# Kernel tuning notes

Measured on AMD Instinct MI355X. Metric: run time of the kernel, lower is better.

Reference implementation:

```python
import jax, jax.numpy as jnp
import numpy as np

SQRT2 = np.float32(np.sqrt(2.0))
D = 256


def setup_inputs() -> dict:
    key = jax.random.key(0)
    k1, = jax.random.split(key, 1)
    x = jax.random.normal(k1, (4, 1024, D), dtype=jnp.float32)
    weight = jnp.ones((D,), dtype=jnp.float32)
    bias = jnp.zeros((D,), dtype=jnp.float32)
    return {"x": x, "weight": weight, "bias": bias}


def reference(x, weight, bias):
    orig_shape = x.shape
    d = orig_shape[-1]
    flat = x.reshape(-1, d)  # [N, D]
    # Silverman 2d bandwidth: 0.9 * std(ddof=1, dim=-1) * D^(-1/5)
    bw = 0.9 * jnp.std(flat, axis=-1, ddof=1) * np.float32(d ** (-0.2))  # [N]
    # Pairwise Gaussian-kernel CDF, averaged over data points (dim 2).
    scaled = (flat[:, :, None] - flat[:, None, :]) / bw[:, None, None]  # [N, D, D]
    cdf = jnp.mean(0.5 * (1.0 + jax.lax.erf(scaled / SQRT2)), axis=2)  # [N, D]
    # Gaussian PPF (inverse CDF)
    normed = jax.lax.erf_inv(2.0 * cdf - 1.0) * SQRT2  # [N, D]
    out = normed.reshape(orig_shape) * weight + bias
    return out
```

## Files before the change

kernel.cpp:

```cpp
#include <hip/hip_runtime.h>
#include <math.h>

#define DD 256
#define NW 4
#define MFIX 24

typedef float v2f __attribute__((ext_vector_type(2)));
typedef float v4f __attribute__((ext_vector_type(4)));

template <int CTRL>
__device__ __forceinline__ float dpp_add(float x) {
    return x + __int_as_float(__builtin_amdgcn_update_dpp(
        0, __float_as_int(x), CTRL, 0xf, 0xf, false));
}
template <int CTRL>
__device__ __forceinline__ float dpp_mov_self(float x) {
    return __int_as_float(__builtin_amdgcn_update_dpp(
        __float_as_int(x), __float_as_int(x), CTRL, 0xf, 0xf, false));
}
__device__ __forceinline__ float wave_sum_chain(float x) {
    x = dpp_add<0x111>(x); x = dpp_add<0x112>(x);
    x = dpp_add<0x114>(x); x = dpp_add<0x118>(x);
    x = dpp_add<0x142>(x); x = dpp_add<0x143>(x);
    return x;
}
__device__ __forceinline__ float lane63(float x) {
    return __int_as_float(__builtin_amdgcn_readlane(__float_as_int(x), 63));
}
__device__ __forceinline__ float wave_max_chain(float x) {
    x = __builtin_fmaxf(x, dpp_mov_self<0x111>(x));
    x = __builtin_fmaxf(x, dpp_mov_self<0x112>(x));
    x = __builtin_fmaxf(x, dpp_mov_self<0x114>(x));
    x = __builtin_fmaxf(x, dpp_mov_self<0x118>(x));
    x = __builtin_fmaxf(x, dpp_mov_self<0x142>(x));
    x = __builtin_fmaxf(x, dpp_mov_self<0x143>(x));
    return x;
}
__device__ __forceinline__ float wave_min_chain(float x) {
    x = __builtin_fminf(x, dpp_mov_self<0x111>(x));
    x = __builtin_fminf(x, dpp_mov_self<0x112>(x));
    x = __builtin_fminf(x, dpp_mov_self<0x114>(x));
    x = __builtin_fminf(x, dpp_mov_self<0x118>(x));
    x = __builtin_fminf(x, dpp_mov_self<0x142>(x));
    x = __builtin_fminf(x, dpp_mov_self<0x143>(x));
    return x;
}

__device__ __forceinline__ float ppf_from_y(float y) {
    float omy2 = __builtin_fmaf(-y, y, 1.0f);
    float wg = __builtin_fmaf(-__builtin_amdgcn_logf(omy2), 0.69314718056f, -2.5f);
    float p = 2.81022636e-08f;
    p = __builtin_fmaf(p, wg, 3.43273939e-07f);
    p = __builtin_fmaf(p, wg, -3.5233877e-06f);
    p = __builtin_fmaf(p, wg, -4.39150654e-06f);
    p = __builtin_fmaf(p, wg, 0.00021858087f);
    p = __builtin_fmaf(p, wg, -0.00125372503f);
    p = __builtin_fmaf(p, wg, -0.00417768164f);
    p = __builtin_fmaf(p, wg, 0.246640727f);
    p = __builtin_fmaf(p, wg, 1.50140941f);
    return p * y * 1.41421356237309505f;
}

__global__ __launch_bounds__(64 * NW, 4) void kd_layernorm_kernel(
        const float* __restrict__ x,
        const float* __restrict__ wgt,
        const float* __restrict__ bia,
        float* __restrict__ out) {
    const int lane = threadIdx.x & 63;
    const int wid  = threadIdx.x >> 6;
    const int row  = blockIdx.x * NW + wid;

    const v4f u = ((const v4f*)(x + (size_t)row * DD))[lane];

    float ssum = lane63(wave_sum_chain((u.x + u.y) + (u.z + u.w)));
    float qsum = lane63(wave_sum_chain(__builtin_fmaf(u.x, u.x, u.y * u.y) +
                                       __builtin_fmaf(u.z, u.z, u.w * u.w)));
    float xmax = lane63(wave_max_chain(__builtin_fmaxf(__builtin_fmaxf(u.x, u.y),
                                                       __builtin_fmaxf(u.z, u.w))));
    float xmin = lane63(wave_min_chain(__builtin_fminf(__builtin_fminf(u.x, u.y),
                                                       __builtin_fminf(u.z, u.w))));

    float var = (qsum - ssum * ssum * (1.0f / DD)) * (1.0f / (DD - 1));
    float bw = 0.9f * __builtin_sqrtf(var) * 0.32987697769322355f;
    float invbw = __builtin_amdgcn_rcpf(bw);
    v4f v = u * invbw;
    float meanv = ssum * invbw * (1.0f / DD);

    float L = (xmax - xmin) * invbw + 10.0f;
    float invL = __builtin_amdgcn_rcpf(L);

    v4f ph = v * invL;
    v4f s1, c1;
    s1.x = __builtin_amdgcn_sinf(ph.x); s1.y = __builtin_amdgcn_sinf(ph.y);
    s1.z = __builtin_amdgcn_sinf(ph.z); s1.w = __builtin_amdgcn_sinf(ph.w);
    c1.x = __builtin_amdgcn_cosf(ph.x); c1.y = __builtin_amdgcn_cosf(ph.y);
    c1.z = __builtin_amdgcn_cosf(ph.z); c1.w = __builtin_amdgcn_cosf(ph.w);

    float PC[MFIX], PS[MFIX];
    {
        v4f sm = s1, cm = c1;
        #pragma unroll
        for (int m = 0; m < MFIX; ++m) {
            PS[m] = (sm.x + sm.y) + (sm.z + sm.w);
            PC[m] = (cm.x + cm.y) + (cm.z + cm.w);
            v4f ns = __builtin_elementwise_fma(sm, c1, cm * s1);
            v4f nc = __builtin_elementwise_fma(cm, c1, -(sm * s1));
            sm = ns; cm = nc;
        }
    }

    {
        float w1sq = 39.4784176044f * invL * invL;
        float g   = __builtin_amdgcn_exp2f(-0.72134752f * w1sq);
        float rr  = __builtin_amdgcn_exp2f(-2.16404256f * w1sq);
        const float rho = __builtin_amdgcn_exp2f(-1.44269504f * w1sq);
        #pragma unroll
        for (int m = 0; m < MFIX; ++m) {
            float Ct = lane63(wave_sum_chain(PC[m]));
            float St = lane63(wave_sum_chain(PS[m]));
            float sc = g * (0.31830988618f / (float)(m + 1));
            PC[m] = Ct * sc;
            PS[m] = St * sc;
            g *= rr; rr *= rho;
        }
    }

    v4f R = {0.f, 0.f, 0.f, 0.f};
    {
        v4f sm = s1, cm = c1;
        #pragma unroll
        for (int m = 0; m < MFIX; ++m) {
            v4f vgC = {PC[m], PC[m], PC[m], PC[m]};
            v4f vgS = {PS[m], PS[m], PS[m], PS[m]};
            R = __builtin_elementwise_fma(sm, vgC, R);
            R = __builtin_elementwise_fma(cm, -vgS, R);
            v4f ns = __builtin_elementwise_fma(sm, c1, cm * s1);
            v4f nc = __builtin_elementwise_fma(cm, c1, -(sm * s1));
            sm = ns; cm = nc;
        }
    }

    const v4f wv = ((const v4f*)wgt)[lane];
    const v4f bv = ((const v4f*)bia)[lane];
    v4f o;
    o.x = __builtin_fmaf(ppf_from_y(2.0f * __builtin_fmaf(v.x - meanv, invL, R.x * (1.0f / DD))), wv.x, bv.x);
    o.y = __builtin_fmaf(ppf_from_y(2.0f * __builtin_fmaf(v.y - meanv, invL, R.y * (1.0f / DD))), wv.y, bv.y);
    o.z = __builtin_fmaf(ppf_from_y(2.0f * __builtin_fmaf(v.z - meanv, invL, R.z * (1.0f / DD))), wv.z, bv.z);
    o.w = __builtin_fmaf(ppf_from_y(2.0f * __builtin_fmaf(v.w - meanv, invL, R.w * (1.0f / DD))), wv.w, bv.w);
    ((v4f*)(out + (size_t)row * DD))[lane] = o;
}

extern "C" void kernel_launch(void* const* d_in, const int* in_sizes, int n_in,
                              void* d_out, int out_size, void* d_ws, size_t ws_size,
                              hipStream_t stream) {
    const float* x = (const float*)d_in[0];
    const float* w = (const float*)d_in[1];
    const float* b = (const float*)d_in[2];
    float* out = (float*)d_out;
    const int nrows = in_sizes[0] / DD;
    kd_layernorm_kernel<<<nrows / NW, 64 * NW, 0, stream>>>(x, w, b, out);
}
```

Measured before the change: 66.70 us.

## Use Chebyshev recurrence for harmonics and fuse reductions in groups for occupancy

Switches the angle-addition rotation for sin/cos harmonics to a Chebyshev three-term recurrence (one FMA per component, using 2cos). The per-harmonic scaling is folded into the first pass and the wave reductions run in groups of 8, so the separate scaling loop disappears and fewer values stay live. The constant factors (2/DD, sign) are also folded into the coefficients, and the launch bound is raised to 6 waves per SIMD to get more occupancy. The recurrence may build up more rounding error over 24 harmonics, and the tighter register budget could cause spills.

```diff
diff --git a/kernel.cpp b/kernel.cpp
--- a/kernel.cpp
+++ b/kernel.cpp
@@ -4,6 +4,7 @@
 #define DD 256
 #define NW 4
 #define MFIX 24
+#define MG 8
 
 typedef float v2f __attribute__((ext_vector_type(2)));
 typedef float v4f __attribute__((ext_vector_type(4)));
@@ -61,7 +62,7 @@
     return p * y * 1.41421356237309505f;
 }
 
-__global__ __launch_bounds__(64 * NW, 4) void kd_layernorm_kernel(
+__global__ __launch_bounds__(64 * NW, 6) void kd_layernorm_kernel(
         const float* __restrict__ x,
         const float* __restrict__ wgt,
         const float* __restrict__ bia,
@@ -95,58 +96,73 @@
     s1.z = __builtin_amdgcn_sinf(ph.z); s1.w = __builtin_amdgcn_sinf(ph.w);
     c1.x = __builtin_amdgcn_cosf(ph.x); c1.y = __builtin_amdgcn_cosf(ph.y);
     c1.z = __builtin_amdgcn_cosf(ph.z); c1.w = __builtin_amdgcn_cosf(ph.w);
+    v4f twoC = c1 + c1;
 
-    float PC[MFIX], PS[MFIX];
+    float w1sq = 39.4784176044f * invL * invL;
+    float g    = __builtin_amdgcn_exp2f(-0.72134752f * w1sq);
+    float rr   = __builtin_amdgcn_exp2f(-2.16404256f * w1sq);
+    const float rho = __builtin_amdgcn_exp2f(-1.44269504f * w1sq);
+
+    float gC[MFIX], gS[MFIX];
     {
         v4f sm = s1, cm = c1;
+        v4f sm1 = {0.f, 0.f, 0.f, 0.f};
+        v4f cm1 = {1.f, 1.f, 1.f, 1.f};
         #pragma unroll
-        for (int m = 0; m < MFIX; ++m) {
-            PS[m] = (sm.x + sm.y) + (sm.z + sm.w);
-            PC[m] = (cm.x + cm.y) + (cm.z + cm.w);
-            v4f ns = __builtin_elementwise_fma(sm, c1, cm * s1);
-            v4f nc = __builtin_elementwise_fma(cm, c1, -(sm * s1));
-            sm = ns; cm = nc;
-        }
-    }
-
-    {
-        float w1sq = 39.4784176044f * invL * invL;
-        float g   = __builtin_amdgcn_exp2f(-0.72134752f * w1sq);
-        float rr  = __builtin_amdgcn_exp2f(-2.16404256f * w1sq);
-        const float rho = __builtin_amdgcn_exp2f(-1.44269504f * w1sq);
-        #pragma unroll
-        for (int m = 0; m < MFIX; ++m) {
-            float Ct = lane63(wave_sum_chain(PC[m]));
-            float St = lane63(wave_sum_chain(PS[m]));
-            float sc = g * (0.31830988618f / (float)(m + 1));
-            PC[m] = Ct * sc;
-            PS[m] = St * sc;
-            g *= rr; rr *= rho;
-        }
-    }
-
-    v4f R = {0.f, 0.f, 0.f, 0.f};
-    {
-        v4f sm = s1, cm = c1;
-        #pragma unroll
-        for (int m = 0; m < MFIX; ++m) {
-            v4f vgC = {PC[m], PC[m], PC[m], PC[m]};
-            v4f vgS = {PS[m], PS[m], PS[m], PS[m]};
-            R = __builtin_elementwise_fma(sm, vgC, R);
-            R = __builtin_elementwise_fma(cm, -vgS, R);
-            v4f ns = __builtin_elementwise_fma(sm, c1, cm * s1);
-            v4f nc = __builtin_elementwise_fma(cm, c1, -(sm * s1));
-            sm = ns; cm = nc;
+        for (int grp = 0; grp < MFIX / MG; ++grp) {
+            float pc[MG], ps[MG];
+            #pragma unroll
+            for (int k = 0; k < MG; ++k) {
+                const int m = grp * MG + k;
+                float sc = g * (0.0024867959f / (float)(m + 1));
+                pc[k] = ((cm.x + cm.y) + (cm.z + cm.w)) * sc;
+                ps[k] = ((sm.x + sm.y) + (sm.z + sm.w)) * (-sc);
+                g *= rr; rr *= rho;
+                v4f sn = __builtin_elementwise_fma(twoC, sm, -sm1);
+                v4f cn = __builtin_elementwise_fma(twoC, cm, -cm1);
+                sm1 = sm; sm = sn;
+                cm1 = cm; cm = cn;
+            }
+            #pragma unroll
+            for (int k = 0; k < MG; ++k) {
+                const int m = grp * MG + k;
+                gC[m] = lane63(wave_sum_chain(pc[k]));
+                gS[m] = lane63(wave_sum_chain(ps[k]));
+            }
         }
     }
 
     const v4f wv = ((const v4f*)wgt)[lane];
     const v4f bv = ((const v4f*)bia)[lane];
+
+    v4f R = {0.f, 0.f, 0.f, 0.f};
+    {
+        v4f sm = s1, cm = c1;
+        v4f sm1 = {0.f, 0.f, 0.f, 0.f};
+        v4f cm1 = {1.f, 1.f, 1.f, 1.f};
+        #pragma unroll
+        for (int m = 0; m < MFIX; ++m) {
+            R.x = __builtin_fmaf(sm.x, gC[m], R.x);
+            R.y = __builtin_fmaf(sm.y, gC[m], R.y);
+            R.z = __builtin_fmaf(sm.z, gC[m], R.z);
+            R.w = __builtin_fmaf(sm.w, gC[m], R.w);
+            R.x = __builtin_fmaf(cm.x, gS[m], R.x);
+            R.y = __builtin_fmaf(cm.y, gS[m], R.y);
+            R.z = __builtin_fmaf(cm.z, gS[m], R.z);
+            R.w = __builtin_fmaf(cm.w, gS[m], R.w);
+            v4f sn = __builtin_elementwise_fma(twoC, sm, -sm1);
+            v4f cn = __builtin_elementwise_fma(twoC, cm, -cm1);
+            sm1 = sm; sm = sn;
+            cm1 = cm; cm = cn;
+        }
+    }
+
+    const float t2iL = invL + invL;
     v4f o;
-    o.x = __builtin_fmaf(ppf_from_y(2.0f * __builtin_fmaf(v.x - meanv, invL, R.x * (1.0f / DD))), wv.x, bv.x);
-    o.y = __builtin_fmaf(ppf_from_y(2.0f * __builtin_fmaf(v.y - meanv, invL, R.y * (1.0f / DD))), wv.y, bv.y);
-    o.z = __builtin_fmaf(ppf_from_y(2.0f * __builtin_fmaf(v.z - meanv, invL, R.z * (1.0f / DD))), wv.z, bv.z);
-    o.w = __builtin_fmaf(ppf_from_y(2.0f * __builtin_fmaf(v.w - meanv, invL, R.w * (1.0f / DD))), wv.w, bv.w);
+    o.x = __builtin_fmaf(ppf_from_y(__builtin_fmaf(v.x - meanv, t2iL, R.x)), wv.x, bv.x);
+    o.y = __builtin_fmaf(ppf_from_y(__builtin_fmaf(v.y - meanv, t2iL, R.y)), wv.y, bv.y);
+    o.z = __builtin_fmaf(ppf_from_y(__builtin_fmaf(v.z - meanv, t2iL, R.z)), wv.z, bv.z);
+    o.w = __builtin_fmaf(ppf_from_y(__builtin_fmaf(v.w - meanv, t2iL, R.w)), wv.w, bv.w);
     ((v4f*)(out + (size_t)row * DD))[lane] = o;
 }
 
```

Measured after the change: 113.4 us. 1.7x slower.
